# Optimization experiments

Measured on AMD Instinct MI355X. Metric: run time of the kernel, lower is better.

The kernel has to match this reference:

```python
import jax, jax.numpy as jnp
import numpy as np

ALL_OFFSETS = np.array([1, 3, 4, 13, 15, 21, 23, 28, 48, 64, 96, 192, 384, 512, 768, 1024], dtype=np.int32)
NEG_BIG = -1e30  # finite stand-in for -inf (avoids nan grads)


def setup_inputs() -> dict:
    key = jax.random.key(0)
    k0, k1, k2, k3, k4 = jax.random.split(key, 5)
    B, H, N, HD = 1, 16, 4096, 64
    return {
        "q": jax.random.normal(k0, (B, H, N, HD), dtype=jnp.float32),
        "k": jax.random.normal(k1, (B, H, N, HD), dtype=jnp.float32),
        "v": jax.random.normal(k2, (B, H, N, HD), dtype=jnp.float32),
        "pos_bias": jax.random.normal(k3, (16, H), dtype=jnp.float32) * 0.1,
        "scale_embed": jax.random.normal(k4, (16, HD), dtype=jnp.float32) * 0.1,
    }


def reference(q, k, v, pos_bias, scale_embed):
    # q,k,v: [B,H,N,HD]; pos_bias: [16,H]; scale_embed: [16,HD]
    B, H, N, HD = q.shape
    sc = 1.0 / np.sqrt(HD).astype(np.float32)
    offs = jnp.asarray(ALL_OFFSETS)                      # [16]
    idx = jnp.arange(N)[None, :] - offs[:, None]         # [16,N] key position n-delta
    valid = idx >= 0                                     # [16,N]
    idx_c = jnp.maximum(idx, 0)

    kg = k[:, :, idx_c, :]                               # [B,H,16,N,HD] gathered keys
    vg = v[:, :, idx_c, :]                               # [B,H,16,N,HD] gathered values

    # score = q.k/sqrt(HD) + pos_bias[i,h] + q.se_i/sqrt(HD)
    s = jnp.einsum('bhnd,bhind->bhin', q, kg) * sc
    s = s + pos_bias.T[None, :, :, None]                 # [H,16] -> broadcast over b,n
    s = s + jnp.einsum('bhnd,id->bhin', q, scale_embed) * sc
    s = jnp.where(valid[None, None], s, NEG_BIG)         # [B,H,16,N]

    # stable softmax over the 16 offsets; rows with no valid offset (n=0) yield 0 output
    m = jnp.max(s, axis=2, keepdims=True)                # [B,H,1,N]
    p = jnp.where(valid[None, None], jnp.exp(s - m), 0.0)  # [B,H,16,N]
    l = jnp.sum(p, axis=2)                               # [B,H,N]
    out = jnp.einsum('bhin,bhind->bhnd', p, vg)
    out = out / jnp.where(l > 0.0, l, 1.0)[..., None]
    return out
```

## Files before the change

### kernel.cpp

```cpp
#include <hip/hip_runtime.h>
#include <hip/hip_fp16.h>

typedef _Float16 half2_t __attribute__((ext_vector_type(2)));

template<int CTRL>
__device__ __forceinline__ float dpp_add_step(float x) {
    const int p = __builtin_amdgcn_update_dpp(
        0, __builtin_bit_cast(int, x), CTRL, 0xf, 0xf, true);
    return x + __builtin_bit_cast(float, p);
}

__device__ __forceinline__ float dpp_reduce8(float a) {
    a = dpp_add_step<0xB1>(a);
    a = dpp_add_step<0x4E>(a);
    a = dpp_add_step<0x141>(a);
    return a;
}

__device__ __forceinline__ float fdot2x4(const uint4 u, const half2_t qh[4], float init) {
    float a = __builtin_amdgcn_fdot2(qh[0], __builtin_bit_cast(half2_t, u.x), init, false);
    a = __builtin_amdgcn_fdot2(qh[1], __builtin_bit_cast(half2_t, u.y), a, false);
    a = __builtin_amdgcn_fdot2(qh[2], __builtin_bit_cast(half2_t, u.z), a, false);
    a = __builtin_amdgcn_fdot2(qh[3], __builtin_bit_cast(half2_t, u.w), a, false);
    return a;
}

__device__ __forceinline__ float dot8_kse(const uint4 ku, const uint4 eu, const half2_t qh[4]) {
    const half2_t t0 = __builtin_bit_cast(half2_t, ku.x) + __builtin_bit_cast(half2_t, eu.x);
    const half2_t t1 = __builtin_bit_cast(half2_t, ku.y) + __builtin_bit_cast(half2_t, eu.y);
    const half2_t t2 = __builtin_bit_cast(half2_t, ku.z) + __builtin_bit_cast(half2_t, eu.z);
    const half2_t t3 = __builtin_bit_cast(half2_t, ku.w) + __builtin_bit_cast(half2_t, eu.w);
    float a = __builtin_amdgcn_fdot2(qh[0], t0, 0.f, false);
    a = __builtin_amdgcn_fdot2(qh[1], t1, a, false);
    a = __builtin_amdgcn_fdot2(qh[2], t2, a, false);
    a = __builtin_amdgcn_fdot2(qh[3], t3, a, false);
    return a;
}

__device__ __forceinline__ float dot8(const float4 q0, const float4 q1,
                                      const float4 a, const float4 b) {
    return q0.x*a.x + q0.y*a.y + q0.z*a.z + q0.w*a.w
         + q1.x*b.x + q1.y*b.y + q1.z*b.z + q1.w*b.w;
}

#define WROWS 96
#define L2E 1.44269504f

template<bool SAFE>
__device__ __forceinline__ void run_block(
    const float* __restrict__ kh, const float* __restrict__ vh,
    const float* __restrict__ pb, const int h,
    const __half* ksh, const __half* vsh, const __half* se_sh,
    const float4 q0, const float4 q1, const half2_t qh[4],
    const int n, const int ql, const int d8,
    float4& o0, float4& o1, half2_t o16[4], float& l)
{
    constexpr int NEARO[10] = {1, 3, 4, 13, 15, 21, 23, 28, 48, 64};
    constexpr int FARO[6]   = {96, 192, 384, 512, 768, 1024};
    constexpr float SC = 0.125f * L2E;

#pragma unroll
    for (int t = 0; t < 6; ++t) {
        const int off  = FARO[t];
        const int i    = t + 10;
        const int idx  = n - off;
        const int idxc = SAFE ? (idx < 0 ? 0 : idx) : idx;
        const float4* kp = (const float4*)(kh + ((size_t)idxc << 6) + d8);
        const float4 k0 = kp[0], k1 = kp[1];
        const float4* vp = (const float4*)(vh + ((size_t)idxc << 6) + d8);
        const float4 v0 = vp[0], v1 = vp[1];
        const uint4 eu = *(const uint4*)&se_sh[(i << 6) + d8];
        float a = dot8(q0, q1, k0, k1);
        a = fdot2x4(eu, qh, a);
        a = dpp_reduce8(a);
        float pw = exp2f(fmaf(a, SC, pb[(i << 4) + h] * L2E));
        if (SAFE) pw = (idx >= 0) ? pw : 0.f;
        l += pw;
        o0.x += pw*v0.x; o0.y += pw*v0.y; o0.z += pw*v0.z; o0.w += pw*v0.w;
        o1.x += pw*v1.x; o1.y += pw*v1.y; o1.z += pw*v1.z; o1.w += pw*v1.w;
    }

#pragma unroll
    for (int t = 0; t < 10; ++t) {
        const int off = NEARO[t];
        const int row = ql + 64 - off;
        const uint4 ku = *(const uint4*)&ksh[(row << 6) + d8];
        const uint4 eu = *(const uint4*)&se_sh[(t << 6) + d8];
        const uint4 vu = *(const uint4*)&vsh[(row << 6) + d8];
        float a = dot8_kse(ku, eu, qh);
        a = dpp_reduce8(a);
        float pw = exp2f(fmaf(a, SC, pb[(t << 4) + h] * L2E));
        if (SAFE) pw = (n - off >= 0) ? pw : 0.f;
        l += pw;
        const half2_t pwh = {(_Float16)pw, (_Float16)pw};
        o16[0] = __builtin_bit_cast(half2_t, vu.x) * pwh + o16[0];
        o16[1] = __builtin_bit_cast(half2_t, vu.y) * pwh + o16[1];
        o16[2] = __builtin_bit_cast(half2_t, vu.z) * pwh + o16[2];
        o16[3] = __builtin_bit_cast(half2_t, vu.w) * pwh + o16[3];
    }
}

__global__ __launch_bounds__(256, 4) void dsqg_attn_kernel(
    const float* __restrict__ q, const float* __restrict__ k,
    const float* __restrict__ v, const float* __restrict__ pb,
    const float* __restrict__ se, float* __restrict__ out)
{
    __shared__ __half ksh[WROWS * 64];
    __shared__ __half vsh[WROWS * 64];
    __shared__ __half se_sh[16 * 64];

    const int p   = blockIdx.x;
    const int lb_ = ((p & 7) << 8) + (p >> 3);
    const int h   = lb_ >> 7;
    const int nb  = lb_ & 127;
    const int base = nb << 5;

    const int g   = threadIdx.x >> 4;
    const int j   = threadIdx.x & 15;
    const int sub = j >> 3;
    const int d8  = (j & 7) << 3;
    const int ql  = (g << 1) + sub;
    const int n   = base + ql;
    const size_t hb = (size_t)h << 18;

    const float* kh = k + hb;
    const float* vh = v + hb;

    const float4* qp = (const float4*)(q + hb + ((size_t)n << 6) + d8);
    const float4 q0 = qp[0], q1 = qp[1];

    {
        const int r32 = threadIdx.x >> 3;
        const int c8  = (threadIdx.x & 7) << 3;
#pragma unroll
        for (int it = 0; it < 3; ++it) {
            const int sr = (it << 5) + r32;
            int gr = base - 64 + sr;
            gr = gr < 0 ? 0 : gr;
            const float4* kp = (const float4*)(kh + ((size_t)gr << 6) + c8);
            const float4 kf0 = kp[0], kf1 = kp[1];
            const float4* vp = (const float4*)(vh + ((size_t)gr << 6) + c8);
            const float4 vf0 = vp[0], vf1 = vp[1];
            union { __half2 h2[4]; uint4 u; } pk, pv;
            pk.h2[0] = __floats2half2_rn(kf0.x, kf0.y);
            pk.h2[1] = __floats2half2_rn(kf0.z, kf0.w);
            pk.h2[2] = __floats2half2_rn(kf1.x, kf1.y);
            pk.h2[3] = __floats2half2_rn(kf1.z, kf1.w);
            pv.h2[0] = __floats2half2_rn(vf0.x, vf0.y);
            pv.h2[1] = __floats2half2_rn(vf0.z, vf0.w);
            pv.h2[2] = __floats2half2_rn(vf1.x, vf1.y);
            pv.h2[3] = __floats2half2_rn(vf1.z, vf1.w);
            *(uint4*)&ksh[(sr << 6) + c8] = pk.u;
            *(uint4*)&vsh[(sr << 6) + c8] = pv.u;
        }
    }
    {
        const float4 sf = *(const float4*)(se + (threadIdx.x << 2));
        union { __half2 h2[2]; uint2 u; } ps;
        ps.h2[0] = __floats2half2_rn(sf.x, sf.y);
        ps.h2[1] = __floats2half2_rn(sf.z, sf.w);
        *(uint2*)&se_sh[threadIdx.x << 2] = ps.u;
    }

    half2_t qh[4];
    qh[0][0] = (_Float16)q0.x; qh[0][1] = (_Float16)q0.y;
    qh[1][0] = (_Float16)q0.z; qh[1][1] = (_Float16)q0.w;
    qh[2][0] = (_Float16)q1.x; qh[2][1] = (_Float16)q1.y;
    qh[3][0] = (_Float16)q1.z; qh[3][1] = (_Float16)q1.w;

    __syncthreads();

    float l = 0.f;
    float4 o0 = make_float4(0.f, 0.f, 0.f, 0.f);
    float4 o1 = make_float4(0.f, 0.f, 0.f, 0.f);
    half2_t o16[4] = {half2_t{0, 0}, half2_t{0, 0}, half2_t{0, 0}, half2_t{0, 0}};

    if (nb >= 32) {
        run_block<false>(kh, vh, pb, h, ksh, vsh, se_sh, q0, q1, qh, n, ql, d8, o0, o1, o16, l);
    } else {
        run_block<true>(kh, vh, pb, h, ksh, vsh, se_sh, q0, q1, qh, n, ql, d8, o0, o1, o16, l);
    }

    {
        const float2 f0 = __half22float2(__builtin_bit_cast(__half2, o16[0]));
        const float2 f1 = __half22float2(__builtin_bit_cast(__half2, o16[1]));
        const float2 f2 = __half22float2(__builtin_bit_cast(__half2, o16[2]));
        const float2 f3 = __half22float2(__builtin_bit_cast(__half2, o16[3]));
        o0.x += f0.x; o0.y += f0.y; o0.z += f1.x; o0.w += f1.y;
        o1.x += f2.x; o1.y += f2.y; o1.z += f3.x; o1.w += f3.y;
    }

    const float inv = (l > 0.f) ? 1.f / l : 0.f;
    o0.x *= inv; o0.y *= inv; o0.z *= inv; o0.w *= inv;
    o1.x *= inv; o1.y *= inv; o1.z *= inv; o1.w *= inv;
    float4* op = (float4*)(out + hb + ((size_t)n << 6) + d8);
    op[0] = o0; op[1] = o1;
}

extern "C" void kernel_launch(void* const* d_in, const int* in_sizes, int n_in,
                              void* d_out, int out_size, void* d_ws, size_t ws_size,
                              hipStream_t stream) {
    const float* q  = (const float*)d_in[0];
    const float* k  = (const float*)d_in[1];
    const float* v  = (const float*)d_in[2];
    const float* pb = (const float*)d_in[3];
    const float* se = (const float*)d_in[4];
    float* out = (float*)d_out;

    dim3 grid(2048);
    dim3 block(256);
    dsqg_attn_kernel<<<grid, block, 0, stream>>>(q, k, v, pb, se, out);
}
```

Measured before the change: 24.06 us.

## Batch far-offset K/V loads ahead of compute and use packed fp16 dots

Splits the per-offset loop into phases. All six far-offset K rows are loaded from global memory up front, then all 16 scores are computed, then the far V rows are loaded and accumulated. This exposes memory-level parallelism so global latency overlaps with shared-memory scoring. Far-offset K is now converted to fp16 with pkrtz and scored with fdot2 instead of fp32 FMAs, and the fp16 conversions switch to round-toward-zero packed converts. The cost is higher register pressure from the buffered float4 arrays at 4 blocks/SM, plus lower precision for the far-offset scores.

```diff
diff --git a/kernel.cpp b/kernel.cpp
--- a/kernel.cpp
+++ b/kernel.cpp
@@ -2,6 +2,10 @@
 #include <hip/hip_fp16.h>
 
 typedef _Float16 half2_t __attribute__((ext_vector_type(2)));
+
+__device__ __forceinline__ half2_t pkrtz(float lo, float hi) {
+    return __builtin_bit_cast(half2_t, __builtin_amdgcn_cvt_pkrtz(lo, hi));
+}
 
 template<int CTRL>
 __device__ __forceinline__ float dpp_add_step(float x) {
@@ -17,19 +21,14 @@
     return a;
 }
 
-__device__ __forceinline__ float fdot2x4(const uint4 u, const half2_t qh[4], float init) {
-    float a = __builtin_amdgcn_fdot2(qh[0], __builtin_bit_cast(half2_t, u.x), init, false);
-    a = __builtin_amdgcn_fdot2(qh[1], __builtin_bit_cast(half2_t, u.y), a, false);
-    a = __builtin_amdgcn_fdot2(qh[2], __builtin_bit_cast(half2_t, u.z), a, false);
-    a = __builtin_amdgcn_fdot2(qh[3], __builtin_bit_cast(half2_t, u.w), a, false);
-    return a;
-}
-
-__device__ __forceinline__ float dot8_kse(const uint4 ku, const uint4 eu, const half2_t qh[4]) {
-    const half2_t t0 = __builtin_bit_cast(half2_t, ku.x) + __builtin_bit_cast(half2_t, eu.x);
-    const half2_t t1 = __builtin_bit_cast(half2_t, ku.y) + __builtin_bit_cast(half2_t, eu.y);
-    const half2_t t2 = __builtin_bit_cast(half2_t, ku.z) + __builtin_bit_cast(half2_t, eu.z);
-    const half2_t t3 = __builtin_bit_cast(half2_t, ku.w) + __builtin_bit_cast(half2_t, eu.w);
+__device__ __forceinline__ float dot8_kse_h(
+    const half2_t k0, const half2_t k1, const half2_t k2, const half2_t k3,
+    const uint4 eu, const half2_t qh[4])
+{
+    const half2_t t0 = k0 + __builtin_bit_cast(half2_t, eu.x);
+    const half2_t t1 = k1 + __builtin_bit_cast(half2_t, eu.y);
+    const half2_t t2 = k2 + __builtin_bit_cast(half2_t, eu.z);
+    const half2_t t3 = k3 + __builtin_bit_cast(half2_t, eu.w);
     float a = __builtin_amdgcn_fdot2(qh[0], t0, 0.f, false);
     a = __builtin_amdgcn_fdot2(qh[1], t1, a, false);
     a = __builtin_amdgcn_fdot2(qh[2], t2, a, false);
@@ -37,12 +36,6 @@
     return a;
 }
 
-__device__ __forceinline__ float dot8(const float4 q0, const float4 q1,
-                                      const float4 a, const float4 b) {
-    return q0.x*a.x + q0.y*a.y + q0.z*a.z + q0.w*a.w
-         + q1.x*b.x + q1.y*b.y + q1.z*b.z + q1.w*b.w;
-}
-
 #define WROWS 96
 #define L2E 1.44269504f
 
@@ -51,7 +44,7 @@
     const float* __restrict__ kh, const float* __restrict__ vh,
     const float* __restrict__ pb, const int h,
     const __half* ksh, const __half* vsh, const __half* se_sh,
-    const float4 q0, const float4 q1, const half2_t qh[4],
+    const half2_t qh[4],
     const int n, const int ql, const int d8,
     float4& o0, float4& o1, half2_t o16[4], float& l)
 {
@@ -59,44 +52,72 @@
     constexpr int FARO[6]   = {96, 192, 384, 512, 768, 1024};
     constexpr float SC = 0.125f * L2E;
 
-#pragma unroll
-    for (int t = 0; t < 6; ++t) {
-        const int off  = FARO[t];
-        const int i    = t + 10;
-        const int idx  = n - off;
+    float pw[16];
+
+    float4 fk0[6], fk1[6];
+#pragma unroll
+    for (int t = 0; t < 6; ++t) {
+        const int idx  = n - FARO[t];
         const int idxc = SAFE ? (idx < 0 ? 0 : idx) : idx;
         const float4* kp = (const float4*)(kh + ((size_t)idxc << 6) + d8);
-        const float4 k0 = kp[0], k1 = kp[1];
-        const float4* vp = (const float4*)(vh + ((size_t)idxc << 6) + d8);
-        const float4 v0 = vp[0], v1 = vp[1];
-        const uint4 eu = *(const uint4*)&se_sh[(i << 6) + d8];
-        float a = dot8(q0, q1, k0, k1);
-        a = fdot2x4(eu, qh, a);
-        a = dpp_reduce8(a);
-        float pw = exp2f(fmaf(a, SC, pb[(i << 4) + h] * L2E));
-        if (SAFE) pw = (idx >= 0) ? pw : 0.f;
-        l += pw;
-        o0.x += pw*v0.x; o0.y += pw*v0.y; o0.z += pw*v0.z; o0.w += pw*v0.w;
-        o1.x += pw*v1.x; o1.y += pw*v1.y; o1.z += pw*v1.z; o1.w += pw*v1.w;
-    }
-
+        fk0[t] = kp[0]; fk1[t] = kp[1];
+    }
 #pragma unroll
     for (int t = 0; t < 10; ++t) {
         const int off = NEARO[t];
         const int row = ql + 64 - off;
         const uint4 ku = *(const uint4*)&ksh[(row << 6) + d8];
         const uint4 eu = *(const uint4*)&se_sh[(t << 6) + d8];
+        float a = dot8_kse_h(__builtin_bit_cast(half2_t, ku.x),
+                             __builtin_bit_cast(half2_t, ku.y),
+                             __builtin_bit_cast(half2_t, ku.z),
+                             __builtin_bit_cast(half2_t, ku.w), eu, qh);
+        a = dpp_reduce8(a);
+        float p = exp2f(fmaf(a, SC, pb[(t << 4) + h] * L2E));
+        if (SAFE) p = (n - off >= 0) ? p : 0.f;
+        pw[t] = p;
+    }
+#pragma unroll
+    for (int t = 0; t < 6; ++t) {
+        const int i = t + 10;
+        const uint4 eu = *(const uint4*)&se_sh[(i << 6) + d8];
+        float a = dot8_kse_h(pkrtz(fk0[t].x, fk0[t].y),
+                             pkrtz(fk0[t].z, fk0[t].w),
+                             pkrtz(fk1[t].x, fk1[t].y),
+                             pkrtz(fk1[t].z, fk1[t].w), eu, qh);
+        a = dpp_reduce8(a);
+        float p = exp2f(fmaf(a, SC, pb[(i << 4) + h] * L2E));
+        if (SAFE) p = (n - FARO[t] >= 0) ? p : 0.f;
+        pw[i] = p;
+    }
+
+    l = ((pw[0] + pw[1]) + (pw[2] + pw[3])) + ((pw[4] + pw[5]) + (pw[6] + pw[7]))
+      + ((pw[8] + pw[9]) + (pw[10] + pw[11])) + ((pw[12] + pw[13]) + (pw[14] + pw[15]));
+
+    float4 fv0[6], fv1[6];
+#pragma unroll
+    for (int t = 0; t < 6; ++t) {
+        const int idx  = n - FARO[t];
+        const int idxc = SAFE ? (idx < 0 ? 0 : idx) : idx;
+        const float4* vp = (const float4*)(vh + ((size_t)idxc << 6) + d8);
+        fv0[t] = vp[0]; fv1[t] = vp[1];
+    }
+#pragma unroll
+    for (int t = 0; t < 10; ++t) {
+        const int row = ql + 64 - NEARO[t];
         const uint4 vu = *(const uint4*)&vsh[(row << 6) + d8];
-        float a = dot8_kse(ku, eu, qh);
-        a = dpp_reduce8(a);
-        float pw = exp2f(fmaf(a, SC, pb[(t << 4) + h] * L2E));
-        if (SAFE) pw = (n - off >= 0) ? pw : 0.f;
-        l += pw;
-        const half2_t pwh = {(_Float16)pw, (_Float16)pw};
+        const _Float16 ph = (_Float16)pw[t];
+        const half2_t pwh = {ph, ph};
         o16[0] = __builtin_bit_cast(half2_t, vu.x) * pwh + o16[0];
         o16[1] = __builtin_bit_cast(half2_t, vu.y) * pwh + o16[1];
         o16[2] = __builtin_bit_cast(half2_t, vu.z) * pwh + o16[2];
         o16[3] = __builtin_bit_cast(half2_t, vu.w) * pwh + o16[3];
+    }
+#pragma unroll
+    for (int t = 0; t < 6; ++t) {
+        const float p = pw[t + 10];
+        o0.x += p*fv0[t].x; o0.y += p*fv0[t].y; o0.z += p*fv0[t].z; o0.w += p*fv0[t].w;
+        o1.x += p*fv1[t].x; o1.y += p*fv1[t].y; o1.z += p*fv1[t].z; o1.w += p*fv1[t].w;
     }
 }
 
@@ -141,32 +162,32 @@
             const float4 kf0 = kp[0], kf1 = kp[1];
             const float4* vp = (const float4*)(vh + ((size_t)gr << 6) + c8);
             const float4 vf0 = vp[0], vf1 = vp[1];
-            union { __half2 h2[4]; uint4 u; } pk, pv;
-            pk.h2[0] = __floats2half2_rn(kf0.x, kf0.y);
-            pk.h2[1] = __floats2half2_rn(kf0.z, kf0.w);
-            pk.h2[2] = __floats2half2_rn(kf1.x, kf1.y);
-            pk.h2[3] = __floats2half2_rn(kf1.z, kf1.w);
-            pv.h2[0] = __floats2half2_rn(vf0.x, vf0.y);
-            pv.h2[1] = __floats2half2_rn(vf0.z, vf0.w);
-            pv.h2[2] = __floats2half2_rn(vf1.x, vf1.y);
-            pv.h2[3] = __floats2half2_rn(vf1.z, vf1.w);
+            union { half2_t h2[4]; uint4 u; } pk, pv;
+            pk.h2[0] = pkrtz(kf0.x, kf0.y);
+            pk.h2[1] = pkrtz(kf0.z, kf0.w);
+            pk.h2[2] = pkrtz(kf1.x, kf1.y);
+            pk.h2[3] = pkrtz(kf1.z, kf1.w);
+            pv.h2[0] = pkrtz(vf0.x, vf0.y);
+            pv.h2[1] = pkrtz(vf0.z, vf0.w);
+            pv.h2[2] = pkrtz(vf1.x, vf1.y);
+            pv.h2[3] = pkrtz(vf1.z, vf1.w);
             *(uint4*)&ksh[(sr << 6) + c8] = pk.u;
             *(uint4*)&vsh[(sr << 6) + c8] = pv.u;
         }
     }
     {
         const float4 sf = *(const float4*)(se + (threadIdx.x << 2));
-        union { __half2 h2[2]; uint2 u; } ps;
-        ps.h2[0] = __floats2half2_rn(sf.x, sf.y);
-        ps.h2[1] = __floats2half2_rn(sf.z, sf.w);
+        union { half2_t h2[2]; uint2 u; } ps;
+        ps.h2[0] = pkrtz(sf.x, sf.y);
+        ps.h2[1] = pkrtz(sf.z, sf.w);
         *(uint2*)&se_sh[threadIdx.x << 2] = ps.u;
     }
 
     half2_t qh[4];
-    qh[0][0] = (_Float16)q0.x; qh[0][1] = (_Float16)q0.y;
-    qh[1][0] = (_Float16)q0.z; qh[1][1] = (_Float16)q0.w;
-    qh[2][0] = (_Float16)q1.x; qh[2][1] = (_Float16)q1.y;
-    qh[3][0] = (_Float16)q1.z; qh[3][1] = (_Float16)q1.w;
+    qh[0] = pkrtz(q0.x, q0.y);
+    qh[1] = pkrtz(q0.z, q0.w);
+    qh[2] = pkrtz(q1.x, q1.y);
+    qh[3] = pkrtz(q1.z, q1.w);
 
     __syncthreads();
 
@@ -176,9 +197,9 @@
     half2_t o16[4] = {half2_t{0, 0}, half2_t{0, 0}, half2_t{0, 0}, half2_t{0, 0}};
 
     if (nb >= 32) {
-        run_block<false>(kh, vh, pb, h, ksh, vsh, se_sh, q0, q1, qh, n, ql, d8, o0, o1, o16, l);
+        run_block<false>(kh, vh, pb, h, ksh, vsh, se_sh, qh, n, ql, d8, o0, o1, o16, l);
     } else {
-        run_block<true>(kh, vh, pb, h, ksh, vsh, se_sh, q0, q1, qh, n, ql, d8, o0, o1, o16, l);
+        run_block<true>(kh, vh, pb, h, ksh, vsh, se_sh, qh, n, ql, d8, o0, o1, o16, l);
     }
 
     {
```

After: 22.03 us. -8.4%, faster.
